# Performance work log

Hardware: AMD Instinct MI355X
Metric: run time of the kernel (lower is better)

The kernel has to match this reference:

```python
import jax, jax.numpy as jnp
import numpy as np

B, T, S = 1, 8, 1024
HID, H = 1152, 16
D = HID // H  # 72
EPS = 1e-6


def rmsnorm(t, gamma):
    # t: [b,t,s,h,d], gamma: [h,d] per-head learnable scale (QKNorm)
    var = jnp.mean(jnp.square(t), axis=-1, keepdims=True)
    return t * jax.lax.rsqrt(var + EPS) * gamma


def setup_inputs() -> dict:
    key = jax.random.key(0)
    ks = jax.random.split(key, 8)
    sc = lambda fan_in: 1.0 / np.sqrt(fan_in)
    x = jax.random.normal(ks[0], (B, T, S, HID), dtype=jnp.float32)
    Wq = jax.random.normal(ks[1], (HID, HID), dtype=jnp.float32) * sc(HID)
    bq = jnp.zeros((HID,), dtype=jnp.float32)
    Wkv = jax.random.normal(ks[2], (HID, 2 * HID), dtype=jnp.float32) * sc(HID)
    bkv = jnp.zeros((2 * HID,), dtype=jnp.float32)
    q_gamma = jnp.ones((H, D), dtype=jnp.float32)
    k_gamma = jnp.ones((H, D), dtype=jnp.float32)
    Wo = jax.random.normal(ks[3], (HID, HID), dtype=jnp.float32) * sc(HID)
    return {"x": x, "Wq": Wq, "bq": bq, "Wkv": Wkv, "bkv": bkv,
            "q_gamma": q_gamma, "k_gamma": k_gamma, "Wo": Wo}


def reference(x, Wq, bq, Wkv, bkv, q_gamma, k_gamma, Wo):
    b, t, s, _ = x.shape
    q = (x @ Wq + bq).reshape(b, t, s, H, D)
    kv = x @ Wkv + bkv
    k, v = jnp.split(kv, 2, axis=-1)
    k = k.reshape(b, t, s, H, D)
    v = v.reshape(b, t, s, H, D)
    q = rmsnorm(q, q_gamma)
    k = rmsnorm(k, k_gamma)
    # NOTE: original applies no 1/sqrt(d) scaling (QKNorm replaces it)
    attn_weight = jnp.einsum('btqhd,btkhd->bthqk', q, k)
    attn = jax.nn.softmax(attn_weight, axis=-1)
    out = jnp.einsum('bthqk,btkhd->btqhd', attn, v).reshape(b, t, s, HID)
    return out @ Wo
```

## Files before the change

kernel.cpp:

```cpp
#include <hip/hip_runtime.h>


typedef __attribute__((ext_vector_type(4))) short s16x4;
typedef __attribute__((ext_vector_type(8))) short s16x8;
typedef __attribute__((ext_vector_type(4))) float f32x4;

__device__ __forceinline__ unsigned short f2b(float x) {
  unsigned u = __float_as_uint(x);
  u += 0x7FFFu + ((u >> 16) & 1u);
  return (unsigned short)(u >> 16);
}
__device__ __forceinline__ float b2f(unsigned short u) {
  return __uint_as_float(((unsigned)u) << 16);
}
__device__ __forceinline__ void gld16(const void* g, void* l) {
  __builtin_amdgcn_global_load_lds(
      (const __attribute__((address_space(1))) void*)g,
      (__attribute__((address_space(3))) void*)l, 16, 0, 0);
}

__global__ __launch_bounds__(256) void cvt_bf16_kernel(const float* __restrict__ in,
                                                       unsigned short* __restrict__ out,
                                                       int n8) {
  int i = blockIdx.x * 256 + threadIdx.x;
  if (i >= n8) return;
  const float4* p = (const float4*)(in + (size_t)i * 8);
  float4 a = p[0], b = p[1];
  s16x8 r;
  r[0] = (short)f2b(a.x); r[1] = (short)f2b(a.y); r[2] = (short)f2b(a.z); r[3] = (short)f2b(a.w);
  r[4] = (short)f2b(b.x); r[5] = (short)f2b(b.y); r[6] = (short)f2b(b.z); r[7] = (short)f2b(b.w);
  *(s16x8*)(out + (size_t)i * 8) = r;
}

__global__ __launch_bounds__(256) void transpose_cvt_kernel(const float* __restrict__ W,
                                                            unsigned short* __restrict__ WT,
                                                            int K, int N) {
  __shared__ float tile[32][33];
  int n0 = blockIdx.x * 32, k0 = blockIdx.y * 32;
  int tx = threadIdx.x, ty = threadIdx.y;
#pragma unroll
  for (int i = 0; i < 4; i++)
    tile[ty + i * 8][tx] = W[(size_t)(k0 + ty + i * 8) * N + n0 + tx];
  __syncthreads();
#pragma unroll
  for (int i = 0; i < 4; i++)
    WT[(size_t)(n0 + ty + i * 8) * K + k0 + tx] = f2b(tile[tx][ty + i * 8]);
}

template <int MODE>
__global__ __launch_bounds__(256) void gemm_bt_kernel(const unsigned short* __restrict__ A,
                                                      const unsigned short* __restrict__ BT,
                                                      const float* __restrict__ biasq,
                                                      const float* __restrict__ biaskv,
                                                      int N, int gx,
                                                      float* __restrict__ outF,
                                                      unsigned short* __restrict__ qn,
                                                      unsigned short* __restrict__ kn,
                                                      unsigned short* __restrict__ vt) {
  constexpr int K = 1152;
  constexpr int NT = K / 32;
  __shared__ __align__(16) unsigned short As[3 * 4096];
  __shared__ __align__(16) unsigned short Bs[3 * 4096];
  int tid = threadIdx.x;
  int lane = tid & 63, wave = tid >> 6;
  int wr = (wave >> 1) * 64, wc = (wave & 1) * 64;
  int l15 = lane & 15, lq = lane >> 4;
  int bid = blockIdx.x;
  int xcd = bid & 7;
  int w = bid >> 3;
  int st = w / 24, inner = w - st * 24;
  int ibx = inner % 3, iby = inner / 3;
  int bx = st * 3 + ibx;
  int by = xcd * 8 + iby;
  int brow = by * 128, bcol = bx * 128;
  const unsigned short* AsrcP[2];
  const unsigned short* BsrcP[2];
  int dst0[2];
#pragma unroll
  for (int i = 0; i < 2; i++) {
    int c = tid + 256 * i;
    int row = c >> 2, j = c & 3;
    int f = (((row >> 1) & 1) << 1) | ((row >> 3) & 1);
    int ch = j ^ f;
    AsrcP[i] = A + (size_t)(brow + row) * K + ch * 8;
    BsrcP[i] = BT + (size_t)(bcol + row) * K + ch * 8;
    dst0[i] = (wave * 64 + 256 * i) * 8;
  }
#define STAGE(KT, BUF)                                          \
  {                                                             \
    int kb = (KT) * 32;                                         \
    gld16(AsrcP[0] + kb, &As[(BUF) * 4096 + dst0[0]]);          \
    gld16(BsrcP[0] + kb, &Bs[(BUF) * 4096 + dst0[0]]);          \
    gld16(AsrcP[1] + kb, &As[(BUF) * 4096 + dst0[1]]);          \
    gld16(BsrcP[1] + kb, &Bs[(BUF) * 4096 + dst0[1]]);          \
  }
  int fr = (((l15 >> 1) & 1) << 1) | ((l15 >> 3) & 1);
  int loff = ((lq >> 1) ^ fr) * 8 + (lq & 1) * 4;
  int hoff = loff ^ 16;
  STAGE(0, 0);
  STAGE(1, 1);
  f32x4 acc[4][4] = {};
  int cur = 0;
  for (int kt = 0; kt < NT; kt++) {
    if (kt < NT - 1)
      asm volatile("s_waitcnt vmcnt(4)\n\ts_barrier" ::: "memory");
    else
      asm volatile("s_waitcnt vmcnt(0)\n\ts_barrier" ::: "memory");
    if (kt + 2 < NT) {
      int nb = (cur == 0) ? 2 : cur - 1;
      STAGE(kt + 2, nb);
    }
    int ab = cur * 4096;
    s16x8 af[4], bf[4];
#pragma unroll
    for (int m = 0; m < 4; m++) {
      int ra = ab + (wr + m * 16 + l15) * 32;
      s16x4 lo = *(const s16x4*)&As[ra + loff];
      s16x4 hi = *(const s16x4*)&As[ra + hoff];
      af[m] = __builtin_shufflevector(lo, hi, 0, 1, 2, 3, 4, 5, 6, 7);
      int rb = ab + (wc + m * 16 + l15) * 32;
      s16x4 blo = *(const s16x4*)&Bs[rb + loff];
      s16x4 bhi = *(const s16x4*)&Bs[rb + hoff];
      bf[m] = __builtin_shufflevector(blo, bhi, 0, 1, 2, 3, 4, 5, 6, 7);
    }
    __builtin_amdgcn_s_setprio(1);
#pragma unroll
    for (int m = 0; m < 4; m++)
#pragma unroll
      for (int n = 0; n < 4; n++)
        acc[m][n] = __builtin_amdgcn_mfma_f32_16x16x32_bf16(af[m], bf[n], acc[m][n], 0, 0, 0);
    __builtin_amdgcn_s_setprio(0);
    cur = (cur == 2) ? 0 : cur + 1;
  }
#undef STAGE
#pragma unroll
  for (int m = 0; m < 4; m++) {
#pragma unroll
    for (int n = 0; n < 4; n++) {
#pragma unroll
      for (int r = 0; r < 4; r++) {
        int grow = brow + wr + m * 16 + lq * 4 + r;
        int gcol = bcol + wc + n * 16 + l15;
        float v = acc[m][n][r];
        if (MODE == 0) {
          outF[(size_t)grow * N + gcol] = v;
        } else {
          v += (gcol < 1152) ? biasq[gcol] : biaskv[gcol - 1152];
          int t = grow >> 10, s = grow & 1023;
          if (gcol < 2304) {
            int c = (gcol < 1152) ? gcol : gcol - 1152;
            int h = c / 72, d = c - h * 72;
            unsigned short* dst = (gcol < 1152) ? qn : kn;
            dst[((size_t)((t * 16 + h) * 1024 + s)) * 96 + d] = f2b(v);
          } else {
            int c = gcol - 2304;
            int h = c / 72, d = c - h * 72;
            vt[((size_t)((t * 16 + h) * 80 + d)) * 1024 + s] = f2b(v);
          }
        }
      }
    }
  }
}

__global__ __launch_bounds__(256) void rmsnorm2_kernel(unsigned short* __restrict__ qn,
                                                       unsigned short* __restrict__ kn,
                                                       const float* __restrict__ qg,
                                                       const float* __restrict__ kg) {
  int r = blockIdx.x * 4 + (threadIdx.x >> 6);
  int isK = r >= 131072;
  int g = isK ? r - 131072 : r;
  unsigned short* buf = isK ? kn : qn;
  const float* gamma = isK ? kg : qg;
  int h = (g >> 10) & 15;
  size_t base = (size_t)g * 96;
  int l = threadIdx.x & 63;
  float e0 = b2f(buf[base + l]);
  float e1 = 0.f;
  if (l < 8) e1 = b2f(buf[base + 64 + l]);
  float ss = e0 * e0 + e1 * e1;
#pragma unroll
  for (int m = 1; m < 64; m <<= 1) ss += __shfl_xor(ss, m);
  float sc = rsqrtf(ss * (1.0f / 72.0f) + 1e-6f);
  buf[base + l] = f2b(e0 * sc * gamma[h * 72 + l]);
  if (l < 32) {
    float v = 0.f;
    if (l < 8) v = e1 * sc * gamma[h * 72 + 64 + l];
    buf[base + 64 + l] = f2b(v);
  }
}

__global__ __launch_bounds__(256) void attn_kernel(const unsigned short* __restrict__ Qn,
                                                   const unsigned short* __restrict__ Kn,
                                                   const unsigned short* __restrict__ VtG,
                                                   unsigned short* __restrict__ att) {
  __shared__ unsigned short Kl[2][64][100];
  __shared__ unsigned short Vt[2][80][76];
  int tid = threadIdx.x;
  int lane = tid & 63, wave = tid >> 6;
  int l15 = lane & 15, lq = lane >> 4, kf = lq * 4;
  int bid = blockIdx.x;
  int orig = (bid & 7) * 256 + (bid >> 3);
  int qb = orig & 15, th = orig >> 4;
  int t = th >> 4, h = th & 15;
  const unsigned short* Q = Qn + (size_t)th * 1024 * 96;
  const unsigned short* Kp = Kn + (size_t)th * 1024 * 96;
  const unsigned short* Vg = VtG + (size_t)th * 80 * 1024;
  int qrow0 = qb * 64 + wave * 16;
  int krow[3], kco[3], vd[3], vco[3];
#pragma unroll
  for (int i = 0; i < 3; i++) {
    int c = tid + i * 256;
    krow[i] = c / 12;
    kco[i] = c - 12 * krow[i];
    int cc = tid + i * 256;
    vd[i] = cc >> 3;
    vco[i] = cc & 7;
  }
  bool v2 = tid < 128;
  s16x8 sk[3], sv[3];
  s16x8 qf[3];
#pragma unroll
  for (int c = 0; c < 3; c++) {
    const unsigned short* p = Q + (size_t)(qrow0 + l15) * 96 + c * 32 + kf;
    s16x4 lo = *(const s16x4*)p;
    s16x4 hi = *(const s16x4*)(p + 16);
    qf[c] = __builtin_shufflevector(lo, hi, 0, 1, 2, 3, 4, 5, 6, 7);
  }
  f32x4 o[5] = {};
  float m_r = -3.0e38f, l_r = 0.f;

#pragma unroll
  for (int i = 0; i < 3; i++)
    sk[i] = *(const s16x8*)(Kp + (size_t)krow[i] * 96 + kco[i] * 8);
#pragma unroll
  for (int i = 0; i < 2; i++)
    sv[i] = *(const s16x8*)(Vg + (size_t)vd[i] * 1024 + vco[i] * 8);
  if (v2) sv[2] = *(const s16x8*)(Vg + (size_t)vd[2] * 1024 + vco[2] * 8);
#pragma unroll
  for (int i = 0; i < 3; i++) *(s16x8*)&Kl[0][krow[i]][kco[i] * 8] = sk[i];
#pragma unroll
  for (int i = 0; i < 2; i++) *(s16x8*)&Vt[0][vd[i]][vco[i] * 8] = sv[i];
  if (v2) *(s16x8*)&Vt[0][vd[2]][vco[2] * 8] = sv[2];

  for (int tt = 0; tt < 16; tt++) {
    __syncthreads();
    int cur = tt & 1;
    if (tt < 15) {
      int kv1 = (tt + 1) * 64;
#pragma unroll
      for (int i = 0; i < 3; i++)
        sk[i] = *(const s16x8*)(Kp + (size_t)(kv1 + krow[i]) * 96 + kco[i] * 8);
#pragma unroll
      for (int i = 0; i < 2; i++)
        sv[i] = *(const s16x8*)(Vg + (size_t)vd[i] * 1024 + kv1 + vco[i] * 8);
      if (v2) sv[2] = *(const s16x8*)(Vg + (size_t)vd[2] * 1024 + kv1 + vco[2] * 8);
    }
    f32x4 st[4];
    __builtin_amdgcn_s_setprio(1);
#pragma unroll
    for (int n = 0; n < 4; n++) {
      f32x4 a = {};
#pragma unroll
      for (int c = 0; c < 3; c++) {
        s16x4 lo = *(const s16x4*)&Kl[cur][n * 16 + l15][c * 32 + kf];
        s16x4 hi = *(const s16x4*)&Kl[cur][n * 16 + l15][c * 32 + kf + 16];
        s16x8 kfr = __builtin_shufflevector(lo, hi, 0, 1, 2, 3, 4, 5, 6, 7);
        a = __builtin_amdgcn_mfma_f32_16x16x32_bf16(kfr, qf[c], a, 0, 0, 0);
      }
      st[n] = a;
    }
    __builtin_amdgcn_s_setprio(0);
    float tmax = st[0][0];
#pragma unroll
    for (int n = 0; n < 4; n++)
#pragma unroll
      for (int r = 0; r < 4; r++) tmax = fmaxf(tmax, st[n][r]);
    tmax = fmaxf(tmax, __shfl_xor(tmax, 16));
    tmax = fmaxf(tmax, __shfl_xor(tmax, 32));
    float mn = fmaxf(m_r, tmax);
    float scale = __expf(m_r - mn);
    m_r = mn;
    float sum = 0.f;
#pragma unroll
    for (int n = 0; n < 4; n++)
#pragma unroll
      for (int r = 0; r < 4; r++) {
        float p = __expf(st[n][r] - mn);
        st[n][r] = p;
        sum += p;
      }
    sum += __shfl_xor(sum, 16);
    sum += __shfl_xor(sum, 32);
    l_r = l_r * scale + sum;
#pragma unroll
    for (int r = 0; r < 4; r++) {
      float scq = __shfl(scale, 4 * lq + r);
#pragma unroll
      for (int v = 0; v < 5; v++) o[v][r] *= scq;
    }
    __builtin_amdgcn_s_setprio(1);
#pragma unroll
    for (int b = 0; b < 2; b++) {
      s16x8 pf;
#pragma unroll
      for (int j = 0; j < 8; j++) pf[j] = (short)f2b(st[2 * b + (j >> 2)][j & 3]);
#pragma unroll
      for (int v = 0; v < 5; v++) {
        s16x4 vlo = *(const s16x4*)&Vt[cur][v * 16 + l15][b * 32 + kf];
        s16x4 vhi = *(const s16x4*)&Vt[cur][v * 16 + l15][b * 32 + kf + 16];
        s16x8 vf = __builtin_shufflevector(vlo, vhi, 0, 1, 2, 3, 4, 5, 6, 7);
        o[v] = __builtin_amdgcn_mfma_f32_16x16x32_bf16(pf, vf, o[v], 0, 0, 0);
      }
    }
    __builtin_amdgcn_s_setprio(0);
    if (tt < 15) {
      int nxt = cur ^ 1;
#pragma unroll
      for (int i = 0; i < 3; i++) *(s16x8*)&Kl[nxt][krow[i]][kco[i] * 8] = sk[i];
#pragma unroll
      for (int i = 0; i < 2; i++) *(s16x8*)&Vt[nxt][vd[i]][vco[i] * 8] = sv[i];
      if (v2) *(s16x8*)&Vt[nxt][vd[2]][vco[2] * 8] = sv[2];
    }
  }
#pragma unroll
  for (int r = 0; r < 4; r++) {
    float inv = 1.0f / __shfl(l_r, 4 * lq + r);
    int qrow = qrow0 + 4 * lq + r;
    size_t rowbase = (size_t)(t * 1024 + qrow) * 1152 + h * 72;
#pragma unroll
    for (int v = 0; v < 5; v++) {
      int d = v * 16 + l15;
      if (d < 72) att[rowbase + d] = f2b(o[v][r] * inv);
    }
  }
}

extern "C" void kernel_launch(void* const* d_in, const int* in_sizes, int n_in,
                              void* d_out, int out_size, void* d_ws, size_t ws_size,
                              hipStream_t stream) {
  const float* x   = (const float*)d_in[0];
  const float* Wq  = (const float*)d_in[1];
  const float* bq  = (const float*)d_in[2];
  const float* Wkv = (const float*)d_in[3];
  const float* bkv = (const float*)d_in[4];
  const float* qg  = (const float*)d_in[5];
  const float* kg  = (const float*)d_in[6];
  const float* Wo  = (const float*)d_in[7];
  float* out = (float*)d_out;

  char* w = (char*)d_ws;
  unsigned short* xb   = (unsigned short*)w; w += (size_t)8192 * 1152 * 2;
  unsigned short* WqT  = (unsigned short*)w; w += (size_t)1152 * 1152 * 2;
  unsigned short* WkvT = (unsigned short*)w; w += (size_t)2304 * 1152 * 2;
  unsigned short* WoT  = (unsigned short*)w; w += (size_t)1152 * 1152 * 2;
  unsigned short* qn   = (unsigned short*)w; w += (size_t)128 * 1024 * 96 * 2;
  unsigned short* kn   = (unsigned short*)w; w += (size_t)128 * 1024 * 96 * 2;
  unsigned short* vt   = (unsigned short*)w; w += (size_t)128 * 80 * 1024 * 2;
  unsigned short* att  = (unsigned short*)w; w += (size_t)8192 * 1152 * 2;

  cvt_bf16_kernel<<<4608, 256, 0, stream>>>(x, xb, 9437184 / 8);
  transpose_cvt_kernel<<<dim3(36, 36), dim3(32, 8), 0, stream>>>(Wq, WqT, 1152, 1152);
  transpose_cvt_kernel<<<dim3(72, 36), dim3(32, 8), 0, stream>>>(Wkv, WkvT, 1152, 2304);
  transpose_cvt_kernel<<<dim3(36, 36), dim3(32, 8), 0, stream>>>(Wo, WoT, 1152, 1152);

  gemm_bt_kernel<3><<<1728, 256, 0, stream>>>(xb, WqT, bq, bkv, 3456, 27, nullptr, qn, kn, vt);
  rmsnorm2_kernel<<<65536, 256, 0, stream>>>(qn, kn, qg, kg);

  attn_kernel<<<2048, 256, 0, stream>>>(qn, kn, vt, att);

  gemm_bt_kernel<0><<<576, 256, 0, stream>>>(att, WoT, nullptr, nullptr, 1152, 9, out, nullptr, nullptr, nullptr);
}
```

Before: 327.8 us.

## Switch GEMMs to 32x32x16 MFMA with K-permuted bf16 operand layouts

The projection GEMMs now use 32x32x16 bf16 MFMA instructions instead of 16x16x32, with a 2x2 accumulator grid per wave and two K sub-steps per 32-wide tile. To let each lane read a single 16-byte LDS vector, the K dimension is permuted consistently in the x conversion, the weight transposes and the attention output writes, since GEMM results are invariant to a shared K permutation. The LDS swizzle is simplified to match. The aim is fewer LDS reads and instructions and higher MFMA throughput. The risk is a different bank-conflict pattern and more complex epilogue indexing.

```diff
diff --git a/kernel.cpp b/kernel.cpp
--- a/kernel.cpp
+++ b/kernel.cpp
@@ -4,6 +4,7 @@
 typedef __attribute__((ext_vector_type(4))) short s16x4;
 typedef __attribute__((ext_vector_type(8))) short s16x8;
 typedef __attribute__((ext_vector_type(4))) float f32x4;
+typedef __attribute__((ext_vector_type(16))) float f32x16;
 
 __device__ __forceinline__ unsigned short f2b(float x) {
   unsigned u = __float_as_uint(x);
@@ -21,15 +22,18 @@
 
 __global__ __launch_bounds__(256) void cvt_bf16_kernel(const float* __restrict__ in,
                                                        unsigned short* __restrict__ out,
-                                                       int n8) {
+                                                       int n16) {
   int i = blockIdx.x * 256 + threadIdx.x;
-  if (i >= n8) return;
-  const float4* p = (const float4*)(in + (size_t)i * 8);
-  float4 a = p[0], b = p[1];
-  s16x8 r;
-  r[0] = (short)f2b(a.x); r[1] = (short)f2b(a.y); r[2] = (short)f2b(a.z); r[3] = (short)f2b(a.w);
-  r[4] = (short)f2b(b.x); r[5] = (short)f2b(b.y); r[6] = (short)f2b(b.z); r[7] = (short)f2b(b.w);
-  *(s16x8*)(out + (size_t)i * 8) = r;
+  if (i >= n16) return;
+  const float4* p = (const float4*)(in + (size_t)i * 16);
+  float4 a = p[0], b = p[1], c = p[2], d = p[3];
+  s16x8 r0, r1;
+  r0[0] = (short)f2b(a.x); r0[1] = (short)f2b(a.y); r0[2] = (short)f2b(a.z); r0[3] = (short)f2b(a.w);
+  r0[4] = (short)f2b(c.x); r0[5] = (short)f2b(c.y); r0[6] = (short)f2b(c.z); r0[7] = (short)f2b(c.w);
+  r1[0] = (short)f2b(b.x); r1[1] = (short)f2b(b.y); r1[2] = (short)f2b(b.z); r1[3] = (short)f2b(b.w);
+  r1[4] = (short)f2b(d.x); r1[5] = (short)f2b(d.y); r1[6] = (short)f2b(d.z); r1[7] = (short)f2b(d.w);
+  *(s16x8*)(out + (size_t)i * 16) = r0;
+  *(s16x8*)(out + (size_t)i * 16 + 8) = r1;
 }
 
 __global__ __launch_bounds__(256) void transpose_cvt_kernel(const float* __restrict__ W,
@@ -42,9 +46,10 @@
   for (int i = 0; i < 4; i++)
     tile[ty + i * 8][tx] = W[(size_t)(k0 + ty + i * 8) * N + n0 + tx];
   __syncthreads();
+  int stx = (tx & 19) | ((tx & 4) << 1) | ((tx & 8) >> 1);
 #pragma unroll
   for (int i = 0; i < 4; i++)
-    WT[(size_t)(n0 + ty + i * 8) * K + k0 + tx] = f2b(tile[tx][ty + i * 8]);
+    WT[(size_t)(n0 + ty + i * 8) * K + k0 + stx] = f2b(tile[tx][ty + i * 8]);
 }
 
 template <int MODE>
@@ -64,7 +69,7 @@
   int tid = threadIdx.x;
   int lane = tid & 63, wave = tid >> 6;
   int wr = (wave >> 1) * 64, wc = (wave & 1) * 64;
-  int l15 = lane & 15, lq = lane >> 4;
+  int l31 = lane & 31, lh = lane >> 5;
   int bid = blockIdx.x;
   int xcd = bid & 7;
   int w = bid >> 3;
@@ -80,8 +85,7 @@
   for (int i = 0; i < 2; i++) {
     int c = tid + 256 * i;
     int row = c >> 2, j = c & 3;
-    int f = (((row >> 1) & 1) << 1) | ((row >> 3) & 1);
-    int ch = j ^ f;
+    int ch = j ^ ((row >> 1) & 3);
     AsrcP[i] = A + (size_t)(brow + row) * K + ch * 8;
     BsrcP[i] = BT + (size_t)(bcol + row) * K + ch * 8;
     dst0[i] = (wave * 64 + 256 * i) * 8;
@@ -94,12 +98,11 @@
     gld16(AsrcP[1] + kb, &As[(BUF) * 4096 + dst0[1]]);          \
     gld16(BsrcP[1] + kb, &Bs[(BUF) * 4096 + dst0[1]]);          \
   }
-  int fr = (((l15 >> 1) & 1) << 1) | ((l15 >> 3) & 1);
-  int loff = ((lq >> 1) ^ fr) * 8 + (lq & 1) * 4;
-  int hoff = loff ^ 16;
+  int fr = (l31 >> 1) & 3;
+  int slotk[2] = {(lh ^ fr) * 8, ((2 + lh) ^ fr) * 8};
   STAGE(0, 0);
   STAGE(1, 1);
-  f32x4 acc[4][4] = {};
+  f32x16 acc[2][2] = {};
   int cur = 0;
   for (int kt = 0; kt < NT; kt++) {
     if (kt < NT - 1)
@@ -111,37 +114,36 @@
       STAGE(kt + 2, nb);
     }
     int ab = cur * 4096;
-    s16x8 af[4], bf[4];
-#pragma unroll
-    for (int m = 0; m < 4; m++) {
-      int ra = ab + (wr + m * 16 + l15) * 32;
-      s16x4 lo = *(const s16x4*)&As[ra + loff];
-      s16x4 hi = *(const s16x4*)&As[ra + hoff];
-      af[m] = __builtin_shufflevector(lo, hi, 0, 1, 2, 3, 4, 5, 6, 7);
-      int rb = ab + (wc + m * 16 + l15) * 32;
-      s16x4 blo = *(const s16x4*)&Bs[rb + loff];
-      s16x4 bhi = *(const s16x4*)&Bs[rb + hoff];
-      bf[m] = __builtin_shufflevector(blo, bhi, 0, 1, 2, 3, 4, 5, 6, 7);
-    }
-    __builtin_amdgcn_s_setprio(1);
-#pragma unroll
-    for (int m = 0; m < 4; m++)
-#pragma unroll
-      for (int n = 0; n < 4; n++)
-        acc[m][n] = __builtin_amdgcn_mfma_f32_16x16x32_bf16(af[m], bf[n], acc[m][n], 0, 0, 0);
-    __builtin_amdgcn_s_setprio(0);
+#pragma unroll
+    for (int kk = 0; kk < 2; kk++) {
+      int so = slotk[kk];
+      s16x8 af[2], bf[2];
+#pragma unroll
+      for (int m = 0; m < 2; m++)
+        af[m] = *(const s16x8*)&As[ab + (wr + m * 32 + l31) * 32 + so];
+#pragma unroll
+      for (int n = 0; n < 2; n++)
+        bf[n] = *(const s16x8*)&Bs[ab + (wc + n * 32 + l31) * 32 + so];
+      __builtin_amdgcn_s_setprio(1);
+#pragma unroll
+      for (int m = 0; m < 2; m++)
+#pragma unroll
+        for (int n = 0; n < 2; n++)
+          acc[m][n] = __builtin_amdgcn_mfma_f32_32x32x16_bf16(af[m], bf[n], acc[m][n], 0, 0, 0);
+      __builtin_amdgcn_s_setprio(0);
+    }
     cur = (cur == 2) ? 0 : cur + 1;
   }
 #undef STAGE
 #pragma unroll
-  for (int m = 0; m < 4; m++) {
-#pragma unroll
-    for (int n = 0; n < 4; n++) {
-#pragma unroll
-      for (int r = 0; r < 4; r++) {
-        int grow = brow + wr + m * 16 + lq * 4 + r;
-        int gcol = bcol + wc + n * 16 + l15;
-        float v = acc[m][n][r];
+  for (int m = 0; m < 2; m++) {
+#pragma unroll
+    for (int n = 0; n < 2; n++) {
+#pragma unroll
+      for (int reg = 0; reg < 16; reg++) {
+        int grow = brow + wr + m * 32 + (reg & 3) + 8 * (reg >> 2) + 4 * lh;
+        int gcol = bcol + wc + n * 32 + l31;
+        float v = acc[m][n][reg];
         if (MODE == 0) {
           outF[(size_t)grow * N + gcol] = v;
         } else {
@@ -327,11 +329,15 @@
   for (int r = 0; r < 4; r++) {
     float inv = 1.0f / __shfl(l_r, 4 * lq + r);
     int qrow = qrow0 + 4 * lq + r;
-    size_t rowbase = (size_t)(t * 1024 + qrow) * 1152 + h * 72;
+    size_t rowbase = (size_t)(t * 1024 + qrow) * 1152;
 #pragma unroll
     for (int v = 0; v < 5; v++) {
       int d = v * 16 + l15;
-      if (d < 72) att[rowbase + d] = f2b(o[v][r] * inv);
+      if (d < 72) {
+        int col = h * 72 + d;
+        int scol = (col & ~12) | ((col & 4) << 1) | ((col & 8) >> 1);
+        att[rowbase + scol] = f2b(o[v][r] * inv);
+      }
     }
   }
 }
@@ -359,7 +365,7 @@
   unsigned short* vt   = (unsigned short*)w; w += (size_t)128 * 80 * 1024 * 2;
   unsigned short* att  = (unsigned short*)w; w += (size_t)8192 * 1152 * 2;
 
-  cvt_bf16_kernel<<<4608, 256, 0, stream>>>(x, xb, 9437184 / 8);
+  cvt_bf16_kernel<<<2304, 256, 0, stream>>>(x, xb, 9437184 / 16);
   transpose_cvt_kernel<<<dim3(36, 36), dim3(32, 8), 0, stream>>>(Wq, WqT, 1152, 1152);
   transpose_cvt_kernel<<<dim3(72, 36), dim3(32, 8), 0, stream>>>(Wkv, WkvT, 1152, 2304);
   transpose_cvt_kernel<<<dim3(36, 36), dim3(32, 8), 0, stream>>>(Wo, WoT, 1152, 1152);
```

Result: faster. 313.3 us (-4.4%).
